# Kernel tuning notes

Hardware: AMD Instinct MI355X
Metric: run time of the kernel (lower is better)

## Reference

```python
import jax, jax.numpy as jnp
import numpy as np

N_NODES = 100000
N_EDGES = 1000000
DIM = 128
N_RELS = 500
N_TIMES = 1000


def setup_inputs() -> dict:
    key = jax.random.key(0)
    ks = jax.random.split(key, 8)
    h = jax.random.normal(ks[0], (N_NODES, DIM), dtype=jnp.float32)
    edge_index = jax.random.randint(ks[1], (2, N_EDGES), 0, N_NODES, dtype=jnp.int64)
    edge_type = jax.random.randint(ks[2], (N_EDGES,), 0, N_RELS, dtype=jnp.int64)
    edge_time = jax.random.randint(ks[3], (N_EDGES,), 0, N_TIMES, dtype=jnp.int64)
    query_rel = 7
    rel_table = jax.random.normal(ks[4], (N_RELS, DIM), dtype=jnp.float32)
    time_table = jax.random.normal(ks[5], (N_TIMES, DIM), dtype=jnp.float32)
    # Linear weights stored as [in, out] so y = x @ W + b
    W1 = jax.random.normal(ks[6], (4 * DIM, DIM), dtype=jnp.float32) * (1.0 / np.sqrt(4 * DIM))
    b1 = jnp.zeros((DIM,), dtype=jnp.float32)
    W2 = jax.random.normal(ks[7], (DIM, 1), dtype=jnp.float32) * (1.0 / np.sqrt(DIM))
    b2 = jnp.zeros((1,), dtype=jnp.float32)
    return {"h": h, "edge_index": edge_index, "edge_type": edge_type,
            "edge_time": edge_time, "query_rel": query_rel,
            "rel_table": rel_table, "time_table": time_table,
            "W1": W1, "b1": b1, "W2": W2, "b2": b2}


def reference(h, edge_index, edge_type, edge_time, query_rel,
              rel_table, time_table, W1, b1, W2, b2):
    src = edge_index[0]                    # [E]
    h_s = h[src]                           # [E, D] gather
    h_r = rel_table[edge_type]             # [E, D] embedding lookup
    h_t = time_table[edge_time]            # [E, D] embedding lookup
    h_rq = jnp.broadcast_to(rel_table[query_rel][None, :], h_s.shape)  # [E, D]
    x = jnp.concatenate([h_s, h_r, h_rq, h_t], axis=1)  # [E, 4D]
    hidden = jax.nn.relu(x @ W1 + b1)      # [E, D]
    alpha = hidden @ W2 + b2               # [E, 1]
    return jax.nn.sigmoid(alpha)[:, 0]     # [E]
```

## Files before the change

kernel.cpp:

```cpp
#include <hip/hip_runtime.h>
#include <hip/hip_fp16.h>
#include <math.h>

#define DIM 128

typedef _Float16 half8 __attribute__((ext_vector_type(8)));
typedef _Float16 half2v __attribute__((ext_vector_type(2)));
typedef float floatx4 __attribute__((ext_vector_type(4)));

__global__ __launch_bounds__(256) void precompute(
    const float* __restrict__ h, const float* __restrict__ rel,
    const float* __restrict__ tim, const int* __restrict__ qrel,
    const float* __restrict__ W1, const float* __restrict__ b1,
    __half* __restrict__ Hh, __half* __restrict__ Rh, __half* __restrict__ Th,
    int n_nodes, int n_rels, int n_times, int nHB, int nRB)
{
    const int tid = threadIdx.x;
    const int b = blockIdx.x;

    const float* A; __half* Out; int M, k0, row0; bool isR = false;
    if (b < nHB)            { A = h;   Out = Hh; M = n_nodes; k0 = 0;   row0 = b * 128; }
    else if (b < nHB + nRB) { A = rel; Out = Rh; M = n_rels;  k0 = 128; row0 = (b - nHB) * 128; isR = true; }
    else                    { A = tim; Out = Th; M = n_times; k0 = 384; row0 = (b - nHB - nRB) * 128; }

    __shared__ _Float16 fragB[32 * 64 * 8];
    __shared__ float c0f[DIM];

    for (int idx4 = tid; idx4 < DIM * DIM / 4; idx4 += 256) {
        const int k = idx4 >> 5;
        const int n0 = (idx4 & 31) * 4;
        const float4 v = *(const float4*)&W1[(size_t)(k0 + k) * DIM + n0];
        const int kc = k >> 5, kr = k & 31, q = kr >> 3, j = kr & 7;
        const float vv[4] = {v.x, v.y, v.z, v.w};
#pragma unroll
        for (int i = 0; i < 4; ++i) {
            const int n = n0 + i, ct = n >> 4, n15 = n & 15;
            fragB[(((ct * 4 + kc) * 64) + (q * 16 + n15)) * 8 + j] = (_Float16)vv[i];
        }
    }
    if (isR && tid < DIM) {
        const int q = qrel[0];
        const float* hq = rel + (size_t)q * DIM;
        float s = b1[tid];
        for (int k = 0; k < DIM; ++k)
            s = fmaf(hq[k], W1[(size_t)(256 + k) * DIM + tid], s);
        c0f[tid] = s;
    }
    __syncthreads();

    const int w = tid >> 6;
    const int lane = tid & 63;
    const int m15 = lane & 15, q = lane >> 4;

    const float* aBase[2];
#pragma unroll
    for (int mt = 0; mt < 2; ++mt) {
        int arow = row0 + w * 32 + mt * 16 + m15;
        if (arow >= M) arow = M - 1;
        aBase[mt] = A + (size_t)arow * DIM + q * 8;
    }

    floatx4 acc[2][8];
#pragma unroll
    for (int mt = 0; mt < 2; ++mt)
#pragma unroll
        for (int ct = 0; ct < 8; ++ct) acc[mt][ct] = (floatx4)0.f;

#pragma unroll
    for (int kc = 0; kc < 4; ++kc) {
        half8 af[2];
#pragma unroll
        for (int mt = 0; mt < 2; ++mt) {
            const float4 a0 = *(const float4*)(aBase[mt] + kc * 32);
            const float4 a1 = *(const float4*)(aBase[mt] + kc * 32 + 4);
            af[mt][0] = (_Float16)a0.x; af[mt][1] = (_Float16)a0.y;
            af[mt][2] = (_Float16)a0.z; af[mt][3] = (_Float16)a0.w;
            af[mt][4] = (_Float16)a1.x; af[mt][5] = (_Float16)a1.y;
            af[mt][6] = (_Float16)a1.z; af[mt][7] = (_Float16)a1.w;
        }
#pragma unroll
        for (int ct = 0; ct < 8; ++ct) {
            const half8 bf = *(half8*)&fragB[(((ct * 4 + kc) * 64) + lane) * 8];
            acc[0][ct] = __builtin_amdgcn_mfma_f32_16x16x32_f16(af[0], bf, acc[0][ct], 0, 0, 0);
            acc[1][ct] = __builtin_amdgcn_mfma_f32_16x16x32_f16(af[1], bf, acc[1][ct], 0, 0, 0);
        }
    }

#pragma unroll
    for (int mt = 0; mt < 2; ++mt)
#pragma unroll
        for (int ct = 0; ct < 8; ++ct) {
            const int col = ct * 16 + m15;
            const float cadd = isR ? c0f[col] : 0.f;
#pragma unroll
            for (int r = 0; r < 4; ++r) {
                const int m = row0 + w * 32 + mt * 16 + q * 4 + r;
                if (m < M)
                    Out[(size_t)m * DIM + col] = (_Float16)(acc[mt][ct][r] + cadd);
            }
        }
}

__device__ __forceinline__ float edot(uint4 hu, uint4 ru, uint4 tu,
                                      const half2v* __restrict__ w2h) {
    union U { uint4 u; half2v h[4]; };
    U H, R, T; H.u = hu; R.u = ru; T.u = tu;
    const half2v z = (half2v)(_Float16)0.f;
    float p = 0.f;
#pragma unroll
    for (int j = 0; j < 4; ++j) {
        half2v s = H.h[j] + R.h[j] + T.h[j];
        s = __builtin_elementwise_max(s, z);
#if __has_builtin(__builtin_amdgcn_fdot2)
        p = __builtin_amdgcn_fdot2(s, w2h[j], p, false);
#else
        p = fmaf((float)s[0], (float)w2h[j][0], p);
        p = fmaf((float)s[1], (float)w2h[j][1], p);
#endif
    }
    return p;
}

__global__ __launch_bounds__(256) void edge_kernel(
    const int* __restrict__ ei, const int* __restrict__ ety,
    const int* __restrict__ eti,
    const __half* __restrict__ Hh, const __half* __restrict__ Rh,
    const __half* __restrict__ Th,
    const float* __restrict__ W2, const float* __restrict__ b2,
    float* __restrict__ out, int E, int nGrpTotal)
{
    const int tid = threadIdx.x;
    const int l = tid & 15;
    int g = blockIdx.x * 16 + (tid >> 4);
    const int nQuad = (E + 3) >> 2;
    if (g >= nQuad) return;

    const float4 wA = ((const float4*)W2)[2 * l];
    const float4 wB = ((const float4*)W2)[2 * l + 1];
    half2v w2h[4];
    w2h[0][0] = (_Float16)wA.x; w2h[0][1] = (_Float16)wA.y;
    w2h[1][0] = (_Float16)wA.z; w2h[1][1] = (_Float16)wA.w;
    w2h[2][0] = (_Float16)wB.x; w2h[2][1] = (_Float16)wB.y;
    w2h[3][0] = (_Float16)wB.z; w2h[3][1] = (_Float16)wB.w;
    const float b2v = b2[0];

    int s[4], r[4], t[4];
#pragma unroll
    for (int i = 0; i < 4; ++i) {
        const int e = min(4 * g + i, E - 1);
        s[i] = ei[e]; r[i] = ety[e]; t[i] = eti[e];
    }

    while (true) {
        const int gn = g + nGrpTotal;
        uint4 hv[4], rv[4], tv[4];
#pragma unroll
        for (int i = 0; i < 4; ++i) {
            hv[i] = ((const uint4*)(Hh + (size_t)s[i] * DIM))[l];
            rv[i] = ((const uint4*)(Rh + (size_t)r[i] * DIM))[l];
            tv[i] = ((const uint4*)(Th + (size_t)t[i] * DIM))[l];
        }
        if (gn < nQuad) {
#pragma unroll
            for (int i = 0; i < 4; ++i) {
                const int e = min(4 * gn + i, E - 1);
                s[i] = ei[e]; r[i] = ety[e]; t[i] = eti[e];
            }
        }
        float p[4];
#pragma unroll
        for (int i = 0; i < 4; ++i)
            p[i] = edot(hv[i], rv[i], tv[i], w2h);
#pragma unroll
        for (int off = 8; off > 0; off >>= 1) {
#pragma unroll
            for (int i = 0; i < 4; ++i)
                p[i] += __shfl_down(p[i], off, 16);
        }
        if (l == 0) {
            const int e0 = 4 * g;
            float4 o;
            o.x = 1.f / (1.f + __expf(-(p[0] + b2v)));
            o.y = 1.f / (1.f + __expf(-(p[1] + b2v)));
            o.z = 1.f / (1.f + __expf(-(p[2] + b2v)));
            o.w = 1.f / (1.f + __expf(-(p[3] + b2v)));
            if (e0 + 3 < E) {
                *(float4*)(out + e0) = o;
            } else {
                const float ov[4] = {o.x, o.y, o.z, o.w};
                for (int i = 0; i < 4 && e0 + i < E; ++i) out[e0 + i] = ov[i];
            }
        }
        if (gn >= nQuad) break;
        g = gn;
    }
}

extern "C" void kernel_launch(void* const* d_in, const int* in_sizes, int n_in,
                              void* d_out, int out_size, void* d_ws, size_t ws_size,
                              hipStream_t stream) {
    const float* h          = (const float*)d_in[0];
    const int*   edge_index = (const int*)d_in[1];
    const int*   edge_type  = (const int*)d_in[2];
    const int*   edge_time  = (const int*)d_in[3];
    const int*   query_rel  = (const int*)d_in[4];
    const float* rel_table  = (const float*)d_in[5];
    const float* time_table = (const float*)d_in[6];
    const float* W1         = (const float*)d_in[7];
    const float* b1         = (const float*)d_in[8];
    const float* W2         = (const float*)d_in[9];
    const float* b2         = (const float*)d_in[10];
    float* out = (float*)d_out;

    const int n_nodes = in_sizes[0] / DIM;
    const int E       = in_sizes[2];
    const int n_rels  = in_sizes[5] / DIM;
    const int n_times = in_sizes[6] / DIM;

    __half* Hh = (__half*)d_ws;
    __half* Rh = Hh + (size_t)n_nodes * DIM;
    __half* Th = Rh + (size_t)n_rels * DIM;

    const int nHB = (n_nodes + 127) / 128;
    const int nRB = (n_rels + 127) / 128;
    const int nTB = (n_times + 127) / 128;

    precompute<<<nHB + nRB + nTB, 256, 0, stream>>>(
        h, rel_table, time_table, query_rel, W1, b1,
        Hh, Rh, Th, n_nodes, n_rels, n_times, nHB, nRB);

    const int nBlk = 2048;
    edge_kernel<<<nBlk, 256, 0, stream>>>(
        edge_index, edge_type, edge_time, Hh, Rh, Th, W2, b2,
        out, E, nBlk * 16);
}
```

Before: 179.7 us.

## Cache relation table in LDS, use atomic work-stealing, and vectorize precompute stores

The edge kernel now runs 256 blocks of 1024 threads. Each block stages the first 512 rows of the fp16 relation table in LDS, so relation lookups read shared memory instead of global memory. Work is handed out dynamically through an atomic counter in the workspace, in chunks of 32 quads, with index prefetch for the next quad. The precompute kernel writes a column-permuted fp16 layout, so each row is stored as one 16-byte vector, and the W2 load is permuted to match. It also builds the W1 fragments directly. The trade-off is large LDS use, which limits each CU to one block of 16 waves, plus an extra memset and per-chunk atomics.

```diff
diff --git a/kernel.cpp b/kernel.cpp
--- a/kernel.cpp
+++ b/kernel.cpp
@@ -7,6 +7,7 @@
 typedef _Float16 half8 __attribute__((ext_vector_type(8)));
 typedef _Float16 half2v __attribute__((ext_vector_type(2)));
 typedef float floatx4 __attribute__((ext_vector_type(4)));
+
 
 __global__ __launch_bounds__(256) void precompute(
     const float* __restrict__ h, const float* __restrict__ rel,
@@ -26,17 +27,17 @@
     __shared__ _Float16 fragB[32 * 64 * 8];
     __shared__ float c0f[DIM];
 
-    for (int idx4 = tid; idx4 < DIM * DIM / 4; idx4 += 256) {
-        const int k = idx4 >> 5;
-        const int n0 = (idx4 & 31) * 4;
-        const float4 v = *(const float4*)&W1[(size_t)(k0 + k) * DIM + n0];
-        const int kc = k >> 5, kr = k & 31, q = kr >> 3, j = kr & 7;
-        const float vv[4] = {v.x, v.y, v.z, v.w};
-#pragma unroll
-        for (int i = 0; i < 4; ++i) {
-            const int n = n0 + i, ct = n >> 4, n15 = n & 15;
-            fragB[(((ct * 4 + kc) * 64) + (q * 16 + n15)) * 8 + j] = (_Float16)vv[i];
-        }
+#pragma unroll
+    for (int it = 0; it < 8; ++it) {
+        const int o = tid + it * 256;
+        const int ctkc = o >> 6, L = o & 63;
+        const int ct = ctkc >> 2, kc = ctkc & 3;
+        const int q = L >> 4, n15 = L & 15;
+        const float* base = W1 + (size_t)(k0 + kc * 32 + q * 8) * DIM + ct * 16 + n15;
+        half8 f;
+#pragma unroll
+        for (int j = 0; j < 8; ++j) f[j] = (_Float16)base[(size_t)j * DIM];
+        *(half8*)&fragB[o * 8] = f;
     }
     if (isR && tid < DIM) {
         const int q = qrel[0];
@@ -86,20 +87,26 @@
         }
     }
 
+    float cadd[8];
+#pragma unroll
+    for (int ct = 0; ct < 8; ++ct) cadd[ct] = isR ? c0f[ct * 16 + m15] : 0.f;
+
 #pragma unroll
     for (int mt = 0; mt < 2; ++mt)
 #pragma unroll
-        for (int ct = 0; ct < 8; ++ct) {
-            const int col = ct * 16 + m15;
-            const float cadd = isR ? c0f[col] : 0.f;
-#pragma unroll
-            for (int r = 0; r < 4; ++r) {
-                const int m = row0 + w * 32 + mt * 16 + q * 4 + r;
-                if (m < M)
-                    Out[(size_t)m * DIM + col] = (_Float16)(acc[mt][ct][r] + cadd);
-            }
-        }
-}
+        for (int r = 0; r < 4; ++r) {
+            const int m = row0 + w * 32 + mt * 16 + q * 4 + r;
+            if (m < M) {
+                half8 hv;
+#pragma unroll
+                for (int ct = 0; ct < 8; ++ct)
+                    hv[ct] = (_Float16)(acc[mt][ct][r] + cadd[ct]);
+                *(half8*)(Out + (size_t)m * DIM + m15 * 8) = hv;
+            }
+        }
+}
+
+#define RLDS_ROWS 512
 
 __device__ __forceinline__ float edot(uint4 hu, uint4 ru, uint4 tu,
                                       const half2v* __restrict__ w2h) {
@@ -121,78 +128,103 @@
     return p;
 }
 
-__global__ __launch_bounds__(256) void edge_kernel(
+__global__ __launch_bounds__(1024) void edge_kernel(
     const int* __restrict__ ei, const int* __restrict__ ety,
     const int* __restrict__ eti,
     const __half* __restrict__ Hh, const __half* __restrict__ Rh,
     const __half* __restrict__ Th,
     const float* __restrict__ W2, const float* __restrict__ b2,
-    float* __restrict__ out, int E, int nGrpTotal)
+    float* __restrict__ out, int E, int n_rels, int* __restrict__ counter)
 {
+    __shared__ __half Rlds[RLDS_ROWS * DIM];
+
     const int tid = threadIdx.x;
-    const int l = tid & 15;
-    int g = blockIdx.x * 16 + (tid >> 4);
+    {
+        const uint4* Rv = (const uint4*)Rh;
+        uint4* Lv = (uint4*)Rlds;
+        for (int i = tid; i < RLDS_ROWS * (DIM / 8); i += 1024) Lv[i] = Rv[i];
+    }
+    __syncthreads();
+
+    const int lane = tid & 63;
+    const int grp = lane >> 4;
+    const int l = lane & 15;
     const int nQuad = (E + 3) >> 2;
-    if (g >= nQuad) return;
-
-    const float4 wA = ((const float4*)W2)[2 * l];
-    const float4 wB = ((const float4*)W2)[2 * l + 1];
+
     half2v w2h[4];
-    w2h[0][0] = (_Float16)wA.x; w2h[0][1] = (_Float16)wA.y;
-    w2h[1][0] = (_Float16)wA.z; w2h[1][1] = (_Float16)wA.w;
-    w2h[2][0] = (_Float16)wB.x; w2h[2][1] = (_Float16)wB.y;
-    w2h[3][0] = (_Float16)wB.z; w2h[3][1] = (_Float16)wB.w;
+#pragma unroll
+    for (int j = 0; j < 4; ++j) {
+        w2h[j][0] = (_Float16)W2[(2 * j) * 16 + l];
+        w2h[j][1] = (_Float16)W2[(2 * j + 1) * 16 + l];
+    }
     const float b2v = b2[0];
 
-    int s[4], r[4], t[4];
-#pragma unroll
-    for (int i = 0; i < 4; ++i) {
-        const int e = min(4 * g + i, E - 1);
-        s[i] = ei[e]; r[i] = ety[e]; t[i] = eti[e];
-    }
-
     while (true) {
-        const int gn = g + nGrpTotal;
-        uint4 hv[4], rv[4], tv[4];
+        int b;
+        if (lane == 0) b = atomicAdd(counter, 32);
+        b = __shfl(b, 0);
+        if (b >= nQuad) break;
+
+        int qd = b + grp;
+        int s[4], r[4], t[4];
 #pragma unroll
         for (int i = 0; i < 4; ++i) {
-            hv[i] = ((const uint4*)(Hh + (size_t)s[i] * DIM))[l];
-            rv[i] = ((const uint4*)(Rh + (size_t)r[i] * DIM))[l];
-            tv[i] = ((const uint4*)(Th + (size_t)t[i] * DIM))[l];
-        }
-        if (gn < nQuad) {
+            const int e = min(4 * qd + i, E - 1);
+            s[i] = ei[e]; r[i] = ety[e]; t[i] = eti[e];
+        }
+
+        for (int it = 0; it < 8; ++it) {
+            const bool valid = qd < nQuad;
+            uint4 hv[4], rv[4], tv[4];
 #pragma unroll
             for (int i = 0; i < 4; ++i) {
-                const int e = min(4 * gn + i, E - 1);
-                s[i] = ei[e]; r[i] = ety[e]; t[i] = eti[e];
-            }
-        }
-        float p[4];
-#pragma unroll
-        for (int i = 0; i < 4; ++i)
-            p[i] = edot(hv[i], rv[i], tv[i], w2h);
-#pragma unroll
-        for (int off = 8; off > 0; off >>= 1) {
+                hv[i] = ((const uint4*)(Hh + (size_t)s[i] * DIM))[l];
+                tv[i] = ((const uint4*)(Th + (size_t)t[i] * DIM))[l];
+                if (r[i] < RLDS_ROWS)
+                    rv[i] = ((const uint4*)(Rlds + (size_t)r[i] * DIM))[l];
+                else
+                    rv[i] = ((const uint4*)(Rh + (size_t)r[i] * DIM))[l];
+            }
+            const int qn = b + (it + 1) * 4 + grp;
+            int s2[4], r2[4], t2[4];
+            if (it < 7) {
+#pragma unroll
+                for (int i = 0; i < 4; ++i) {
+                    const int e = min(4 * qn + i, E - 1);
+                    s2[i] = ei[e]; r2[i] = ety[e]; t2[i] = eti[e];
+                }
+            }
+
+            float p[4];
 #pragma unroll
             for (int i = 0; i < 4; ++i)
-                p[i] += __shfl_down(p[i], off, 16);
-        }
-        if (l == 0) {
-            const int e0 = 4 * g;
-            float4 o;
-            o.x = 1.f / (1.f + __expf(-(p[0] + b2v)));
-            o.y = 1.f / (1.f + __expf(-(p[1] + b2v)));
-            o.z = 1.f / (1.f + __expf(-(p[2] + b2v)));
-            o.w = 1.f / (1.f + __expf(-(p[3] + b2v)));
-            if (e0 + 3 < E) {
-                *(float4*)(out + e0) = o;
-            } else {
-                const float ov[4] = {o.x, o.y, o.z, o.w};
-                for (int i = 0; i < 4 && e0 + i < E; ++i) out[e0 + i] = ov[i];
-            }
-        }
-        if (gn >= nQuad) break;
-        g = gn;
+                p[i] = edot(hv[i], rv[i], tv[i], w2h);
+#pragma unroll
+            for (int off = 8; off > 0; off >>= 1) {
+#pragma unroll
+                for (int i = 0; i < 4; ++i)
+                    p[i] += __shfl_down(p[i], off, 16);
+            }
+            if (valid && l == 0) {
+                const int e0 = 4 * qd;
+                float4 o;
+                o.x = 1.f / (1.f + __expf(-(p[0] + b2v)));
+                o.y = 1.f / (1.f + __expf(-(p[1] + b2v)));
+                o.z = 1.f / (1.f + __expf(-(p[2] + b2v)));
+                o.w = 1.f / (1.f + __expf(-(p[3] + b2v)));
+                if (e0 + 3 < E) {
+                    *(float4*)(out + e0) = o;
+                } else {
+                    const float ov[4] = {o.x, o.y, o.z, o.w};
+                    for (int i = 0; i < 4 && e0 + i < E; ++i) out[e0 + i] = ov[i];
+                }
+            }
+            if (it < 7) {
+#pragma unroll
+                for (int i = 0; i < 4; ++i) { s[i] = s2[i]; r[i] = r2[i]; t[i] = t2[i]; }
+            }
+            qd = qn;
+        }
     }
 }
 
@@ -220,6 +252,11 @@
     __half* Hh = (__half*)d_ws;
     __half* Rh = Hh + (size_t)n_nodes * DIM;
     __half* Th = Rh + (size_t)n_rels * DIM;
+    size_t tbl_bytes = ((size_t)(n_nodes + n_rels + n_times) * DIM) * sizeof(__half);
+    tbl_bytes = (tbl_bytes + 255) & ~(size_t)255;
+    int* counter = (int*)((char*)d_ws + tbl_bytes);
+
+    hipMemsetAsync(counter, 0, sizeof(int), stream);
 
     const int nHB = (n_nodes + 127) / 128;
     const int nRB = (n_rels + 127) / 128;
@@ -229,8 +266,7 @@
         h, rel_table, time_table, query_rel, W1, b1,
         Hh, Rh, Th, n_nodes, n_rels, n_times, nHB, nRB);
 
-    const int nBlk = 2048;
-    edge_kernel<<<nBlk, 256, 0, stream>>>(
+    edge_kernel<<<256, 1024, 0, stream>>>(
         edge_index, edge_type, edge_time, Hh, Rh, Th, W2, b2,
-        out, E, nBlk * 16);
-}
+        out, E, n_rels, counter);
+}
```

New measurement: 282.9 us. 1.57x slower.

## Store projected node features as fp8 e4m3 and vectorize precompute stores

Applied to the files above, without the earlier changes.

The per-node projected hidden vectors (h @ W1 slice) are now stored as fp8 e4m3 instead of fp16, with the output columns permuted so each lane holds 8 contiguous bytes. This halves the bytes gathered per edge for the node term, the dominant random-access traffic in the edge kernel. The W2 layout is permuted to match, and the precompute stores become wide vector writes with a rewritten W1 fragment load. The trade-off is a loss of precision in the node projection, which could exceed the output tolerance.

```diff
diff --git a/kernel.cpp b/kernel.cpp
--- a/kernel.cpp
+++ b/kernel.cpp
@@ -1,5 +1,6 @@
 #include <hip/hip_runtime.h>
 #include <hip/hip_fp16.h>
+#include <hip/hip_fp8.h>
 #include <math.h>
 
 #define DIM 128
@@ -7,36 +8,42 @@
 typedef _Float16 half8 __attribute__((ext_vector_type(8)));
 typedef _Float16 half2v __attribute__((ext_vector_type(2)));
 typedef float floatx4 __attribute__((ext_vector_type(4)));
+
+
+__device__ __forceinline__ unsigned char enc_fp8(float x) {
+    return __hip_fp8_e4m3(x).__x;
+}
 
 __global__ __launch_bounds__(256) void precompute(
     const float* __restrict__ h, const float* __restrict__ rel,
     const float* __restrict__ tim, const int* __restrict__ qrel,
     const float* __restrict__ W1, const float* __restrict__ b1,
-    __half* __restrict__ Hh, __half* __restrict__ Rh, __half* __restrict__ Th,
+    unsigned char* __restrict__ H8, __half* __restrict__ Rh, __half* __restrict__ Th,
     int n_nodes, int n_rels, int n_times, int nHB, int nRB)
 {
     const int tid = threadIdx.x;
     const int b = blockIdx.x;
 
-    const float* A; __half* Out; int M, k0, row0; bool isR = false;
-    if (b < nHB)            { A = h;   Out = Hh; M = n_nodes; k0 = 0;   row0 = b * 128; }
-    else if (b < nHB + nRB) { A = rel; Out = Rh; M = n_rels;  k0 = 128; row0 = (b - nHB) * 128; isR = true; }
-    else                    { A = tim; Out = Th; M = n_times; k0 = 384; row0 = (b - nHB - nRB) * 128; }
+    const float* A; int M, k0, row0; bool isR = false, isH = false;
+    __half* Out = nullptr;
+    if (b < nHB)            { A = h;   isH = true; M = n_nodes; k0 = 0;   row0 = b * 128; }
+    else if (b < nHB + nRB) { A = rel; Out = Rh;   M = n_rels;  k0 = 128; row0 = (b - nHB) * 128; isR = true; }
+    else                    { A = tim; Out = Th;   M = n_times; k0 = 384; row0 = (b - nHB - nRB) * 128; }
 
     __shared__ _Float16 fragB[32 * 64 * 8];
     __shared__ float c0f[DIM];
 
-    for (int idx4 = tid; idx4 < DIM * DIM / 4; idx4 += 256) {
-        const int k = idx4 >> 5;
-        const int n0 = (idx4 & 31) * 4;
-        const float4 v = *(const float4*)&W1[(size_t)(k0 + k) * DIM + n0];
-        const int kc = k >> 5, kr = k & 31, q = kr >> 3, j = kr & 7;
-        const float vv[4] = {v.x, v.y, v.z, v.w};
-#pragma unroll
-        for (int i = 0; i < 4; ++i) {
-            const int n = n0 + i, ct = n >> 4, n15 = n & 15;
-            fragB[(((ct * 4 + kc) * 64) + (q * 16 + n15)) * 8 + j] = (_Float16)vv[i];
-        }
+#pragma unroll
+    for (int it = 0; it < 8; ++it) {
+        const int o = tid + it * 256;
+        const int ctkc = o >> 6, L = o & 63;
+        const int ct = ctkc >> 2, kc = ctkc & 3;
+        const int q = L >> 4, n15 = L & 15;
+        const float* base = W1 + (size_t)(k0 + kc * 32 + q * 8) * DIM + ct * 16 + n15;
+        half8 f;
+#pragma unroll
+        for (int j = 0; j < 8; ++j) f[j] = (_Float16)base[(size_t)j * DIM];
+        *(half8*)&fragB[o * 8] = f;
     }
     if (isR && tid < DIM) {
         const int q = qrel[0];
@@ -86,30 +93,56 @@
         }
     }
 
+    float cadd[8];
+#pragma unroll
+    for (int ct = 0; ct < 8; ++ct) cadd[ct] = isR ? c0f[ct * 16 + m15] : 0.f;
+
 #pragma unroll
     for (int mt = 0; mt < 2; ++mt)
 #pragma unroll
-        for (int ct = 0; ct < 8; ++ct) {
-            const int col = ct * 16 + m15;
-            const float cadd = isR ? c0f[col] : 0.f;
-#pragma unroll
-            for (int r = 0; r < 4; ++r) {
-                const int m = row0 + w * 32 + mt * 16 + q * 4 + r;
-                if (m < M)
-                    Out[(size_t)m * DIM + col] = (_Float16)(acc[mt][ct][r] + cadd);
+        for (int r = 0; r < 4; ++r) {
+            const int m = row0 + w * 32 + mt * 16 + q * 4 + r;
+            if (m < M) {
+                if (isH) {
+                    union { uint2 u; unsigned char bb[8]; } pk;
+#pragma unroll
+                    for (int ct = 0; ct < 8; ++ct)
+                        pk.bb[ct] = enc_fp8(acc[mt][ct][r]);
+                    *(uint2*)(H8 + (size_t)m * DIM + m15 * 8) = pk.u;
+                } else {
+                    half8 hv;
+#pragma unroll
+                    for (int ct = 0; ct < 8; ++ct)
+                        hv[ct] = (_Float16)(acc[mt][ct][r] + cadd[ct]);
+                    *(half8*)(Out + (size_t)m * DIM + m15 * 8) = hv;
+                }
             }
         }
 }
 
-__device__ __forceinline__ float edot(uint4 hu, uint4 ru, uint4 tu,
+__device__ __forceinline__ half2v fp8x2_to_h2(unsigned u16) {
+#if __has_builtin(__builtin_amdgcn_cvt_pk_f16_fp8)
+    auto c = __builtin_amdgcn_cvt_pk_f16_fp8((short)u16);
+    half2v r; r[0] = c[0]; r[1] = c[1];
+    return r;
+#else
+    auto f = __builtin_amdgcn_cvt_pk_f32_fp8((int)u16, false);
+    half2v r; r[0] = (_Float16)f[0]; r[1] = (_Float16)f[1];
+    return r;
+#endif
+}
+
+__device__ __forceinline__ float edot(uint2 hu, uint4 ru, uint4 tu,
                                       const half2v* __restrict__ w2h) {
     union U { uint4 u; half2v h[4]; };
-    U H, R, T; H.u = hu; R.u = ru; T.u = tu;
+    U R, T; R.u = ru; T.u = tu;
     const half2v z = (half2v)(_Float16)0.f;
+    const unsigned hw[4] = {hu.x & 0xffffu, hu.x >> 16, hu.y & 0xffffu, hu.y >> 16};
     float p = 0.f;
 #pragma unroll
     for (int j = 0; j < 4; ++j) {
-        half2v s = H.h[j] + R.h[j] + T.h[j];
+        const half2v hh = fp8x2_to_h2(hw[j]);
+        half2v s = hh + R.h[j] + T.h[j];
         s = __builtin_elementwise_max(s, z);
 #if __has_builtin(__builtin_amdgcn_fdot2)
         p = __builtin_amdgcn_fdot2(s, w2h[j], p, false);
@@ -124,7 +157,7 @@
 __global__ __launch_bounds__(256) void edge_kernel(
     const int* __restrict__ ei, const int* __restrict__ ety,
     const int* __restrict__ eti,
-    const __half* __restrict__ Hh, const __half* __restrict__ Rh,
+    const unsigned char* __restrict__ H8, const __half* __restrict__ Rh,
     const __half* __restrict__ Th,
     const float* __restrict__ W2, const float* __restrict__ b2,
     float* __restrict__ out, int E, int nGrpTotal)
@@ -135,13 +168,12 @@
     const int nQuad = (E + 3) >> 2;
     if (g >= nQuad) return;
 
-    const float4 wA = ((const float4*)W2)[2 * l];
-    const float4 wB = ((const float4*)W2)[2 * l + 1];
     half2v w2h[4];
-    w2h[0][0] = (_Float16)wA.x; w2h[0][1] = (_Float16)wA.y;
-    w2h[1][0] = (_Float16)wA.z; w2h[1][1] = (_Float16)wA.w;
-    w2h[2][0] = (_Float16)wB.x; w2h[2][1] = (_Float16)wB.y;
-    w2h[3][0] = (_Float16)wB.z; w2h[3][1] = (_Float16)wB.w;
+#pragma unroll
+    for (int j = 0; j < 4; ++j) {
+        w2h[j][0] = (_Float16)W2[(2 * j) * 16 + l];
+        w2h[j][1] = (_Float16)W2[(2 * j + 1) * 16 + l];
+    }
     const float b2v = b2[0];
 
     int s[4], r[4], t[4];
@@ -153,10 +185,10 @@
 
     while (true) {
         const int gn = g + nGrpTotal;
-        uint4 hv[4], rv[4], tv[4];
+        uint2 hv[4]; uint4 rv[4], tv[4];
 #pragma unroll
         for (int i = 0; i < 4; ++i) {
-            hv[i] = ((const uint4*)(Hh + (size_t)s[i] * DIM))[l];
+            hv[i] = ((const uint2*)(H8 + (size_t)s[i] * DIM))[l];
             rv[i] = ((const uint4*)(Rh + (size_t)r[i] * DIM))[l];
             tv[i] = ((const uint4*)(Th + (size_t)t[i] * DIM))[l];
         }
@@ -217,8 +249,8 @@
     const int n_rels  = in_sizes[5] / DIM;
     const int n_times = in_sizes[6] / DIM;
 
-    __half* Hh = (__half*)d_ws;
-    __half* Rh = Hh + (size_t)n_nodes * DIM;
+    unsigned char* H8 = (unsigned char*)d_ws;
+    __half* Rh = (__half*)(H8 + ((size_t)n_nodes * DIM + 255 & ~(size_t)255));
     __half* Th = Rh + (size_t)n_rels * DIM;
 
     const int nHB = (n_nodes + 127) / 128;
@@ -227,10 +259,10 @@
 
     precompute<<<nHB + nRB + nTB, 256, 0, stream>>>(
         h, rel_table, time_table, query_rel, W1, b1,
-        Hh, Rh, Th, n_nodes, n_rels, n_times, nHB, nRB);
+        H8, Rh, Th, n_nodes, n_rels, n_times, nHB, nRB);
 
     const int nBlk = 2048;
     edge_kernel<<<nBlk, 256, 0, stream>>>(
-        edge_index, edge_type, edge_time, Hh, Rh, Th, W2, b2,
+        edge_index, edge_type, edge_time, H8, Rh, Th, W2, b2,
         out, E, nBlk * 16);
 }
```

Result: faster. 162.7 us (-9.4%).
